# Kernel optimization log

Hardware: AMD Instinct MI355X
Metric: run time of the kernel (lower is better)

The kernel has to match this reference:

```python
import jax, jax.numpy as jnp
import numpy as np

ALPHA = 1.0
EPS = 1e-12  # tf.nn.l2_normalize epsilon


def setup_inputs() -> dict:
    key = jax.random.key(0)
    k1, k2 = jax.random.split(key)
    B, I, J, D, K = 32, 32, 32, 128, 64
    features = jax.random.normal(k1, (B, I, J, D), dtype=jnp.float32)
    kmeans_centers = jax.random.normal(k2, (B, K, D), dtype=jnp.float32)
    return {"features": features, "kmeans_centers": kmeans_centers}


def reference(features, kmeans_centers):
    # features: (B, I, J, D); kmeans_centers: (B, K, D)
    B = features.shape[0]
    # Squared distance ||f - c||^2 expanded to avoid materializing (B,I,J,K,D)
    f2 = jnp.sum(features * features, axis=-1)[..., None]          # (B,I,J,1)
    c2 = jnp.sum(kmeans_centers * kmeans_centers, axis=-1)[:, None, None, :]  # (B,1,1,K)
    fc = jnp.einsum('bijd,bkd->bijk', features, kmeans_centers)     # (B,I,J,K)
    d2 = f2 - 2.0 * fc + c2                                         # (B,I,J,K)
    sim = jax.nn.softmax(-ALPHA * d2, axis=-1)                      # (B,I,J,K)
    # vlad[b,k,d] = sum_ij sim[b,i,j,k] * (f[b,i,j,d] - c[b,k,d])
    vlad = (jnp.einsum('bijk,bijd->bkd', sim, features)
            - jnp.sum(sim, axis=(1, 2))[..., None] * kmeans_centers)  # (B,K,D)
    flat = vlad.reshape(B, -1)                                      # (B, K*D)
    # K.l2_normalize with axis=None -> normalize over ALL elements (global norm)
    norm = jnp.sqrt(jnp.maximum(jnp.sum(flat * flat), EPS))
    return flat / norm
```

## Files before the change

### kernel.cpp

```cpp
#include <hip/hip_runtime.h>
#include <hip/hip_bf16.h>


#define NB    32
#define SPLIT 16

typedef short short8 __attribute__((ext_vector_type(8)));
typedef float f32x4  __attribute__((ext_vector_type(4)));

__device__ __forceinline__ float bf2f(unsigned short u) {
    return __uint_as_float(((unsigned)u) << 16);
}
__device__ __forceinline__ unsigned short f2bf(float f) {
    __hip_bfloat16 h = __float2bfloat16(f);
    unsigned short u;
    __builtin_memcpy(&u, &h, 2);
    return u;
}
__device__ __forceinline__ int swz3(int x) { return (x ^ (x >> 3)) & 7; }

__global__ __launch_bounds__(256)
void netvlad_prep(const float* __restrict__ cent,
                  ushort4* __restrict__ cws,
                  float* __restrict__ c2G) {
    const int tid = threadIdx.x;
    const int bi  = blockIdx.x;
    const int b   = bi >> 3;
    const int kg  = bi & 7;
    const int kk  = tid >> 5;
    const int d4  = tid & 31;
    const int k   = kg * 8 + kk;
    float4 v = ((const float4*)cent)[(size_t)b * 2048 + k * 32 + d4];
    ushort4 h, l;
    h.x = f2bf(v.x); l.x = f2bf(v.x - bf2f(h.x));
    h.y = f2bf(v.y); l.y = f2bf(v.y - bf2f(h.y));
    h.z = f2bf(v.z); l.z = f2bf(v.z - bf2f(h.z));
    h.w = f2bf(v.w); l.w = f2bf(v.w - bf2f(h.w));
    int slot = k * 32 + (d4 ^ ((k & 7) << 1));
    cws[(size_t)b * 4096 + slot]        = h;
    cws[(size_t)b * 4096 + 2048 + slot] = l;
    float a = v.x * v.x + v.y * v.y + v.z * v.z + v.w * v.w;
    a += __shfl_xor(a, 1);
    a += __shfl_xor(a, 2);
    a += __shfl_xor(a, 4);
    a += __shfl_xor(a, 8);
    a += __shfl_xor(a, 16);
    if (d4 == 0) c2G[b * 64 + k] = a;
}

__global__ __launch_bounds__(256, 2)
void netvlad_main(const float* __restrict__ feat,
                  const ushort4* __restrict__ cws,
                  const float* __restrict__ c2G,
                  float* __restrict__ partial,
                  float* __restrict__ ssumG)
{
    __shared__ __align__(16) char smem[58368];
    unsigned short* FT    = (unsigned short*)(smem + 32768);
    unsigned short* ST    = (unsigned short*)(smem + 49152);
    float*          ssumW = (float*)(smem + 57344);

    const int tid = threadIdx.x;
    const int bs  = blockIdx.x;
    const int b   = bs >> 4;
    const int n0  = (bs & 15) * 64;

    const uint4* csrc = (const uint4*)(cws + (size_t)b * 4096);
    #pragma unroll
    for (int it = 0; it < 8; ++it)
        ((uint4*)smem)[it * 256 + tid] = csrc[it * 256 + tid];

    const float4* feat4 = (const float4*)feat + ((size_t)b * 1024 + n0) * 32;

    const int w    = tid >> 6;
    const int lane = tid & 63;
    const int lr   = lane & 15;
    const int lg   = lane >> 4;
    const int prow = 16 * w + lr;

    float c2r[4];
    #pragma unroll
    for (int nt = 0; nt < 4; ++nt) c2r[nt] = c2G[b * 64 + nt * 16 + lr];

    short8 ah[4], al[4];
    #pragma unroll
    for (int kt = 0; kt < 4; ++kt) {
        float4 fa = feat4[prow * 32 + kt * 8 + 2 * lg + 0];
        float4 fb = feat4[prow * 32 + kt * 8 + 2 * lg + 1];
        float fv[8] = { fa.x, fa.y, fa.z, fa.w, fb.x, fb.y, fb.z, fb.w };
        #pragma unroll
        for (int j = 0; j < 8; ++j) {
            unsigned short h = f2bf(fv[j]);
            ah[kt][j] = (short)h;
            al[kt][j] = (short)f2bf(fv[j] - bf2f(h));
            int d = kt * 32 + 8 * lg + j;
            FT[d * 64 + ((((prow >> 3) ^ swz3(d))) << 3) + (prow & 7)] = h;
        }
    }
    __syncthreads();

    f32x4 acc[4];
    #pragma unroll
    for (int nt = 0; nt < 4; ++nt) acc[nt] = (f32x4){0.f, 0.f, 0.f, 0.f};
    #pragma unroll
    for (int kt = 0; kt < 4; ++kt) {
        #pragma unroll
        for (int nt = 0; nt < 4; ++nt) {
            int c  = nt * 16 + lr;
            int ch = c * 16 + ((kt * 4 + lg) ^ (c & 7));
            short8 bh = *(const short8*)(smem + ch * 16);
            short8 bl = *(const short8*)(smem + 16384 + ch * 16);
            acc[nt] = __builtin_amdgcn_mfma_f32_16x16x32_bf16(ah[kt], bh, acc[nt], 0, 0, 0);
            acc[nt] = __builtin_amdgcn_mfma_f32_16x16x32_bf16(ah[kt], bl, acc[nt], 0, 0, 0);
            acc[nt] = __builtin_amdgcn_mfma_f32_16x16x32_bf16(al[kt], bh, acc[nt], 0, 0, 0);
        }
    }

    float ssp[4] = {0.f, 0.f, 0.f, 0.f};
    #pragma unroll
    for (int r = 0; r < 4; ++r) {
        float s[4];
        #pragma unroll
        for (int nt = 0; nt < 4; ++nt) s[nt] = 2.f * acc[nt][r] - c2r[nt];
        float m = fmaxf(fmaxf(s[0], s[1]), fmaxf(s[2], s[3]));
        #pragma unroll
        for (int o = 8; o >= 1; o >>= 1) m = fmaxf(m, __shfl_xor(m, o));
        float e[4], t = 0.f;
        #pragma unroll
        for (int nt = 0; nt < 4; ++nt) { e[nt] = __expf(s[nt] - m); t += e[nt]; }
        #pragma unroll
        for (int o = 8; o >= 1; o >>= 1) t += __shfl_xor(t, o);
        float inv = __builtin_amdgcn_rcpf(t);
        int p = 16 * w + 4 * lg + r;
        #pragma unroll
        for (int nt = 0; nt < 4; ++nt) {
            int k = nt * 16 + lr;
            float val = e[nt] * inv;
            ssp[nt] += val;
            ST[k * 64 + ((((p >> 3) ^ swz3(k))) << 3) + (p & 7)] = f2bf(val);
        }
    }
    #pragma unroll
    for (int nt = 0; nt < 4; ++nt) {
        float v = ssp[nt];
        v += __shfl_xor(v, 16);
        v += __shfl_xor(v, 32);
        if (lg == 0) ssumW[w * 64 + nt * 16 + lr] = v;
    }
    __syncthreads();

    if (tid < 64)
        ssumG[bs * 64 + tid] = ssumW[tid] + ssumW[64 + tid] + ssumW[128 + tid] + ssumW[192 + tid];

    f32x4 vac[8];
    #pragma unroll
    for (int dt = 0; dt < 8; ++dt) vac[dt] = (f32x4){0.f, 0.f, 0.f, 0.f};
    const int krow = 16 * w + lr;
    #pragma unroll
    for (int ks = 0; ks < 2; ++ks) {
        int cA = (ks * 4 + lg) ^ swz3(krow);
        short8 af = *(const short8*)(ST + krow * 64 + (cA << 3));
        #pragma unroll
        for (int dt = 0; dt < 8; ++dt) {
            int d  = dt * 16 + lr;
            int cB = (ks * 4 + lg) ^ swz3(d);
            short8 bf = *(const short8*)(FT + d * 64 + (cB << 3));
            vac[dt] = __builtin_amdgcn_mfma_f32_16x16x32_bf16(af, bf, vac[dt], 0, 0, 0);
        }
    }

    float* outp = partial + (size_t)bs * 8192;
    #pragma unroll
    for (int r = 0; r < 4; ++r) {
        int k = 16 * w + 4 * lg + r;
        #pragma unroll
        for (int dt = 0; dt < 8; ++dt)
            outp[k * 128 + dt * 16 + lr] = vac[dt][r];
    }
}

__global__ __launch_bounds__(256)
void netvlad_reduce(const float* __restrict__ partial,
                    const float* __restrict__ cent,
                    const float* __restrict__ ssumG,
                    float* __restrict__ vlad,
                    float* __restrict__ sqpart) {
    __shared__ float wsum[4];
    int idx = blockIdx.x * 256 + threadIdx.x;
    int b   = idx >> 11;
    int rem = idx & 2047;
    int k   = rem >> 5;
    const float4* p4 = (const float4*)partial;
    float4 a = make_float4(0.f, 0.f, 0.f, 0.f);
    float  ss = 0.f;
    #pragma unroll
    for (int s = 0; s < SPLIT; ++s) {
        float4 v = p4[((size_t)(b * SPLIT + s)) * 2048 + rem];
        a.x += v.x; a.y += v.y; a.z += v.z; a.w += v.w;
        ss += ssumG[(b * SPLIT + s) * 64 + k];
    }
    float4 c4 = ((const float4*)cent)[b * 2048 + rem];
    a.x -= ss * c4.x; a.y -= ss * c4.y; a.z -= ss * c4.z; a.w -= ss * c4.w;
    ((float4*)vlad)[idx] = a;
    float sq = a.x * a.x + a.y * a.y + a.z * a.z + a.w * a.w;
    #pragma unroll
    for (int o = 32; o >= 1; o >>= 1) sq += __shfl_xor(sq, o);
    if ((threadIdx.x & 63) == 0) wsum[threadIdx.x >> 6] = sq;
    __syncthreads();
    if (threadIdx.x == 0) sqpart[blockIdx.x] = wsum[0] + wsum[1] + wsum[2] + wsum[3];
}

__global__ __launch_bounds__(256)
void netvlad_norm(const float* __restrict__ vlad,
                  const float* __restrict__ sqpart,
                  float* __restrict__ out) {
    const float4* sq4 = (const float4*)sqpart;
    float4 v = sq4[threadIdx.x & 63];
    float t = v.x + v.y + v.z + v.w;
    #pragma unroll
    for (int o = 32; o >= 1; o >>= 1) t += __shfl_xor(t, o);
    float inv = __builtin_amdgcn_rcpf(sqrtf(fmaxf(t, 1e-12f)));
    int idx = blockIdx.x * 256 + threadIdx.x;
    float4 x = ((const float4*)vlad)[idx];
    ((float4*)out)[idx] = make_float4(x.x * inv, x.y * inv, x.z * inv, x.w * inv);
}

extern "C" void kernel_launch(void* const* d_in, const int* in_sizes, int n_in,
                              void* d_out, int out_size, void* d_ws, size_t ws_size,
                              hipStream_t stream) {
    const float* feat = (const float*)d_in[0];
    const float* cent = (const float*)d_in[1];
    float* out = (float*)d_out;

    char* ws = (char*)d_ws;
    const size_t partial_bytes = (size_t)NB * SPLIT * 64 * 128 * sizeof(float);
    const size_t cws_bytes     = (size_t)NB * 4096 * sizeof(ushort4);
    const size_t c2_bytes      = (size_t)NB * 64 * sizeof(float);
    const size_t vlad_bytes    = (size_t)NB * 64 * 128 * sizeof(float);
    const size_t ssum_bytes    = (size_t)NB * SPLIT * 64 * sizeof(float);

    float*   partial = (float*)ws;
    ushort4* cwsp    = (ushort4*)(ws + partial_bytes);
    float*   c2G     = (float*)(ws + partial_bytes + cws_bytes);
    float*   vlad    = (float*)(ws + partial_bytes + cws_bytes + c2_bytes);
    float*   ssumG   = (float*)(ws + partial_bytes + cws_bytes + c2_bytes + vlad_bytes);
    float*   sqpart  = (float*)(ws + partial_bytes + cws_bytes + c2_bytes + vlad_bytes + ssum_bytes);

    netvlad_prep  <<<256, 256, 0, stream>>>(cent, cwsp, c2G);
    netvlad_main  <<<NB * SPLIT, 256, 0, stream>>>(feat, cwsp, c2G, partial, ssumG);
    netvlad_reduce<<<256, 256, 0, stream>>>(partial, cent, ssumG, vlad, sqpart);
    netvlad_norm  <<<256, 256, 0, stream>>>(vlad, sqpart, out);
}
```

Before: 79.87 us.

## Accumulate VLAD via atomics and fuse reduce+norm with a grid barrier

The main kernel now atomically adds its per-split VLAD contributions and soft-assignment sums straight into a zeroed VLAD buffer, replacing the large partial buffer and the 16-way reduce pass. The prep kernel zeroes these accumulators. The reduce and normalize kernels are merged into one finish kernel that gathers the global squared norm with an atomic and a spin-wait counter barrier across all 256 blocks. This removes one launch and a lot of partial-buffer traffic, at the cost of heavy float atomic contention, non-deterministic summation order, and a grid barrier that assumes all 256 blocks are resident at once.

```diff
diff --git a/kernel.cpp b/kernel.cpp
--- a/kernel.cpp
+++ b/kernel.cpp
@@ -22,7 +22,11 @@
 __global__ __launch_bounds__(256)
 void netvlad_prep(const float* __restrict__ cent,
                   ushort4* __restrict__ cws,
-                  float* __restrict__ c2G) {
+                  float* __restrict__ c2G,
+                  float* __restrict__ vlad,
+                  float* __restrict__ ssumG,
+                  float* __restrict__ sqG,
+                  unsigned int* __restrict__ ctr) {
     const int tid = threadIdx.x;
     const int bi  = blockIdx.x;
     const int b   = bi >> 3;
@@ -46,13 +50,17 @@
     a += __shfl_xor(a, 8);
     a += __shfl_xor(a, 16);
     if (d4 == 0) c2G[b * 64 + k] = a;
+
+    ((float4*)vlad)[bi * 256 + tid] = make_float4(0.f, 0.f, 0.f, 0.f);
+    if (bi < 8) ssumG[bi * 256 + tid] = 0.f;
+    if (bi == 0 && tid == 0) { sqG[0] = 0.f; ctr[0] = 0u; }
 }
 
 __global__ __launch_bounds__(256, 2)
 void netvlad_main(const float* __restrict__ feat,
                   const ushort4* __restrict__ cws,
                   const float* __restrict__ c2G,
-                  float* __restrict__ partial,
+                  float* __restrict__ vlad,
                   float* __restrict__ ssumG)
 {
     __shared__ __align__(16) char smem[58368];
@@ -149,8 +157,10 @@
     }
     __syncthreads();
 
-    if (tid < 64)
-        ssumG[bs * 64 + tid] = ssumW[tid] + ssumW[64 + tid] + ssumW[128 + tid] + ssumW[192 + tid];
+    if (tid < 64) {
+        float s = ssumW[tid] + ssumW[64 + tid] + ssumW[128 + tid] + ssumW[192 + tid];
+        atomicAdd(&ssumG[b * 64 + tid], s);
+    }
 
     f32x4 vac[8];
     #pragma unroll
@@ -169,60 +179,51 @@
         }
     }
 
-    float* outp = partial + (size_t)bs * 8192;
+    float* vb = vlad + (size_t)b * 8192;
     #pragma unroll
     for (int r = 0; r < 4; ++r) {
         int k = 16 * w + 4 * lg + r;
         #pragma unroll
         for (int dt = 0; dt < 8; ++dt)
-            outp[k * 128 + dt * 16 + lr] = vac[dt][r];
+            atomicAdd(&vb[k * 128 + dt * 16 + lr], vac[dt][r]);
     }
 }
 
 __global__ __launch_bounds__(256)
-void netvlad_reduce(const float* __restrict__ partial,
+void netvlad_finish(const float* __restrict__ vlad,
                     const float* __restrict__ cent,
                     const float* __restrict__ ssumG,
-                    float* __restrict__ vlad,
-                    float* __restrict__ sqpart) {
+                    float* __restrict__ sqG,
+                    unsigned int* __restrict__ ctr,
+                    float* __restrict__ out) {
     __shared__ float wsum[4];
-    int idx = blockIdx.x * 256 + threadIdx.x;
+    const int tid = threadIdx.x;
+    int idx = blockIdx.x * 256 + tid;
     int b   = idx >> 11;
     int rem = idx & 2047;
     int k   = rem >> 5;
-    const float4* p4 = (const float4*)partial;
-    float4 a = make_float4(0.f, 0.f, 0.f, 0.f);
-    float  ss = 0.f;
-    #pragma unroll
-    for (int s = 0; s < SPLIT; ++s) {
-        float4 v = p4[((size_t)(b * SPLIT + s)) * 2048 + rem];
-        a.x += v.x; a.y += v.y; a.z += v.z; a.w += v.w;
-        ss += ssumG[(b * SPLIT + s) * 64 + k];
-    }
+    float4 a  = ((const float4*)vlad)[idx];
+    float  ss = ssumG[b * 64 + k];
     float4 c4 = ((const float4*)cent)[b * 2048 + rem];
     a.x -= ss * c4.x; a.y -= ss * c4.y; a.z -= ss * c4.z; a.w -= ss * c4.w;
-    ((float4*)vlad)[idx] = a;
+
     float sq = a.x * a.x + a.y * a.y + a.z * a.z + a.w * a.w;
     #pragma unroll
     for (int o = 32; o >= 1; o >>= 1) sq += __shfl_xor(sq, o);
-    if ((threadIdx.x & 63) == 0) wsum[threadIdx.x >> 6] = sq;
-    __syncthreads();
-    if (threadIdx.x == 0) sqpart[blockIdx.x] = wsum[0] + wsum[1] + wsum[2] + wsum[3];
-}
-
-__global__ __launch_bounds__(256)
-void netvlad_norm(const float* __restrict__ vlad,
-                  const float* __restrict__ sqpart,
-                  float* __restrict__ out) {
-    const float4* sq4 = (const float4*)sqpart;
-    float4 v = sq4[threadIdx.x & 63];
-    float t = v.x + v.y + v.z + v.w;
-    #pragma unroll
-    for (int o = 32; o >= 1; o >>= 1) t += __shfl_xor(t, o);
+    if ((tid & 63) == 0) wsum[tid >> 6] = sq;
+    __syncthreads();
+    if (tid == 0) {
+        atomicAdd(sqG, wsum[0] + wsum[1] + wsum[2] + wsum[3]);
+        __threadfence();
+        atomicAdd(ctr, 1u);
+        while (__hip_atomic_load(ctr, __ATOMIC_ACQUIRE, __HIP_MEMORY_SCOPE_AGENT) < 256u)
+            __builtin_amdgcn_s_sleep(8);
+    }
+    __syncthreads();
+
+    float t = __hip_atomic_load(sqG, __ATOMIC_RELAXED, __HIP_MEMORY_SCOPE_AGENT);
     float inv = __builtin_amdgcn_rcpf(sqrtf(fmaxf(t, 1e-12f)));
-    int idx = blockIdx.x * 256 + threadIdx.x;
-    float4 x = ((const float4*)vlad)[idx];
-    ((float4*)out)[idx] = make_float4(x.x * inv, x.y * inv, x.z * inv, x.w * inv);
+    ((float4*)out)[idx] = make_float4(a.x * inv, a.y * inv, a.z * inv, a.w * inv);
 }
 
 extern "C" void kernel_launch(void* const* d_in, const int* in_sizes, int n_in,
@@ -233,21 +234,19 @@
     float* out = (float*)d_out;
 
     char* ws = (char*)d_ws;
-    const size_t partial_bytes = (size_t)NB * SPLIT * 64 * 128 * sizeof(float);
-    const size_t cws_bytes     = (size_t)NB * 4096 * sizeof(ushort4);
-    const size_t c2_bytes      = (size_t)NB * 64 * sizeof(float);
-    const size_t vlad_bytes    = (size_t)NB * 64 * 128 * sizeof(float);
-    const size_t ssum_bytes    = (size_t)NB * SPLIT * 64 * sizeof(float);
-
-    float*   partial = (float*)ws;
-    ushort4* cwsp    = (ushort4*)(ws + partial_bytes);
-    float*   c2G     = (float*)(ws + partial_bytes + cws_bytes);
-    float*   vlad    = (float*)(ws + partial_bytes + cws_bytes + c2_bytes);
-    float*   ssumG   = (float*)(ws + partial_bytes + cws_bytes + c2_bytes + vlad_bytes);
-    float*   sqpart  = (float*)(ws + partial_bytes + cws_bytes + c2_bytes + vlad_bytes + ssum_bytes);
-
-    netvlad_prep  <<<256, 256, 0, stream>>>(cent, cwsp, c2G);
-    netvlad_main  <<<NB * SPLIT, 256, 0, stream>>>(feat, cwsp, c2G, partial, ssumG);
-    netvlad_reduce<<<256, 256, 0, stream>>>(partial, cent, ssumG, vlad, sqpart);
-    netvlad_norm  <<<256, 256, 0, stream>>>(vlad, sqpart, out);
-}
+    const size_t cws_bytes  = (size_t)NB * 4096 * sizeof(ushort4);
+    const size_t c2_bytes   = (size_t)NB * 64 * sizeof(float);
+    const size_t vlad_bytes = (size_t)NB * 64 * 128 * sizeof(float);
+    const size_t ssum_bytes = (size_t)NB * 64 * sizeof(float);
+
+    ushort4*      cwsp  = (ushort4*)ws;
+    float*        c2G   = (float*)(ws + cws_bytes);
+    float*        vlad  = (float*)(ws + cws_bytes + c2_bytes);
+    float*        ssumG = (float*)(ws + cws_bytes + c2_bytes + vlad_bytes);
+    float*        sqG   = (float*)(ws + cws_bytes + c2_bytes + vlad_bytes + ssum_bytes);
+    unsigned int* ctr   = (unsigned int*)(ws + cws_bytes + c2_bytes + vlad_bytes + ssum_bytes + 256);
+
+    netvlad_prep  <<<256, 256, 0, stream>>>(cent, cwsp, c2G, vlad, ssumG, sqG, ctr);
+    netvlad_main  <<<NB * SPLIT, 256, 0, stream>>>(feat, cwsp, c2G, vlad, ssumG);
+    netvlad_finish<<<256, 256, 0, stream>>>(vlad, cent, ssumG, sqG, ctr, out);
+}
```

Measured after the change: 101.3 us. +26.8%, slower.
